# Kernel optimization log

Measured on AMD Instinct MI355X. Metric: run time of the kernel, lower is better.

Reference implementation:

```python
import jax, jax.numpy as jnp
import numpy as np

N_FEATURES = 32
HIDDEN_DIM = 64
B, T = 512, 1024


def lstm(x, w_ih, w_hh, b_ih, b_hh):
    """PyTorch-compatible single-layer LSTM, batch_first.
    x: [B, T, F_in]; w_ih: [4H, F_in]; w_hh: [4H, H]; b_ih, b_hh: [4H].
    Gate order (PyTorch): i, f, g, o. Returns outputs [B, T, H].
    """
    Bq, Tq, _ = x.shape
    H = w_hh.shape[1]
    # Precompute input contribution for all timesteps (big GEMM, time-parallel)
    x_gates = jnp.einsum('btf,gf->btg', x, w_ih) + b_ih + b_hh  # [B, T, 4H]
    x_gates = jnp.swapaxes(x_gates, 0, 1)  # [T, B, 4H]

    def step(carry, xg):
        h, c = carry
        gates = xg + h @ w_hh.T  # [B, 4H]
        i = jax.nn.sigmoid(gates[:, 0 * H:1 * H])
        f = jax.nn.sigmoid(gates[:, 1 * H:2 * H])
        g = jnp.tanh(gates[:, 2 * H:3 * H])
        o = jax.nn.sigmoid(gates[:, 3 * H:4 * H])
        c = f * c + i * g
        h = o * jnp.tanh(c)
        return (h, c), h

    h0 = jnp.zeros((Bq, H), dtype=x.dtype)
    c0 = jnp.zeros((Bq, H), dtype=x.dtype)
    _, hs = jax.lax.scan(step, (h0, c0), x_gates)  # hs: [T, B, H]
    return jnp.swapaxes(hs, 0, 1)  # [B, T, H]


def setup_inputs() -> dict:
    key = jax.random.key(0)
    ks = jax.random.split(key, 9)
    F, H = N_FEATURES, HIDDEN_DIM
    s_enc = 1.0 / np.sqrt(H)
    s_dec = 1.0 / np.sqrt(F)
    return {
        'x': jax.random.normal(ks[0], (B, T, F), dtype=jnp.float32),
        # encoder: input F -> hidden H
        'enc_w_ih': jax.random.uniform(ks[1], (4 * H, F), jnp.float32, -s_enc, s_enc),
        'enc_w_hh': jax.random.uniform(ks[2], (4 * H, H), jnp.float32, -s_enc, s_enc),
        'enc_b_ih': jax.random.uniform(ks[3], (4 * H,), jnp.float32, -s_enc, s_enc),
        'enc_b_hh': jax.random.uniform(ks[4], (4 * H,), jnp.float32, -s_enc, s_enc),
        # decoder: input H -> hidden F
        'dec_w_ih': jax.random.uniform(ks[5], (4 * F, H), jnp.float32, -s_dec, s_dec),
        'dec_w_hh': jax.random.uniform(ks[6], (4 * F, F), jnp.float32, -s_dec, s_dec),
        'dec_b_ih': jax.random.uniform(ks[7], (4 * F,), jnp.float32, -s_dec, s_dec),
        'dec_b_hh': jax.random.uniform(ks[8], (4 * F,), jnp.float32, -s_dec, s_dec),
    }


def reference(x, enc_w_ih, enc_w_hh, enc_b_ih, enc_b_hh,
              dec_w_ih, dec_w_hh, dec_b_ih, dec_b_hh):
    encoded = lstm(x, enc_w_ih, enc_w_hh, enc_b_ih, enc_b_hh)      # [B, T, H]
    decoded = lstm(encoded, dec_w_ih, dec_w_hh, dec_b_ih, dec_b_hh)  # [B, T, F]
    return decoded
```

## Files before the change

kernel.cpp:

```cpp
#include <hip/hip_runtime.h>
#include <stdint.h>
#include <math.h>

#define TT 1024
#define FF 32
#define HH 64

typedef unsigned int u32;
typedef _Float16 f16;
typedef __attribute__((ext_vector_type(8))) _Float16 half8;
typedef __attribute__((ext_vector_type(4))) float v4f;

__device__ __forceinline__ float fsig(float x) {
    return __builtin_amdgcn_rcpf(1.f + __builtin_amdgcn_exp2f(-1.44269504088896341f * x));
}
__device__ __forceinline__ float ftanh(float x) {
    return 2.f * __builtin_amdgcn_rcpf(1.f + __builtin_amdgcn_exp2f(-2.88539008177792681f * x)) - 1.f;
}

__device__ __forceinline__ half8 ld8h(const float* p) {
    float4 a = *(const float4*)p, b = *(const float4*)(p + 4);
    half8 r;
    r[0] = (f16)a.x; r[1] = (f16)a.y; r[2] = (f16)a.z; r[3] = (f16)a.w;
    r[4] = (f16)b.x; r[5] = (f16)b.y; r[6] = (f16)b.z; r[7] = (f16)b.w;
    return r;
}


__global__ __launch_bounds__(256, 2)
void lstm_ae_mfma(const float* __restrict__ x,
                  const float* __restrict__ ewih, const float* __restrict__ ewhh,
                  const float* __restrict__ ebih, const float* __restrict__ ebhh,
                  const float* __restrict__ dwih, const float* __restrict__ dwhh,
                  const float* __restrict__ dbih, const float* __restrict__ dbhh,
                  float* __restrict__ out)
{
    const int b = blockIdx.x;
    const int t = threadIdx.x;
    const int w = t >> 6;
    const int l = t & 63;
    const int q = l >> 4;
    const int n = l & 15;

    __shared__ __align__(16) f16 Bst[2][2][160];
    __shared__ __align__(16) float xst[2][2048];

    half8 af[6][3];
#pragma unroll
    for (int i = 0; i < 6; ++i) {
        int tile = w * 6 + i;
        if (tile < 16) {
            int r = (n & 3) * 64 + tile * 4 + (n >> 2);
            af[i][0] = ld8h(ewhh + r * 64 + q * 8);
            af[i][1] = ld8h(ewhh + r * 64 + 32 + q * 8);
            af[i][2] = ld8h(ewih + r * 32 + q * 8);
        } else {
            int r = (n & 3) * 32 + (tile - 16) * 4 + (n >> 2);
            af[i][0] = ld8h(dwih + r * 64 + q * 8);
            af[i][1] = ld8h(dwih + r * 64 + 32 + q * 8);
            af[i][2] = ld8h(dwhh + r * 32 + q * 8);
        }
    }

    const int sel = n >> 1;
    const bool act = (n < 12);
    const int tile_s = w * 6 + (sel < 6 ? sel : 0);
    const bool is_enc = (tile_s < 16);
    const int u = is_enc ? (tile_s * 4 + q) : ((tile_s - 16) * 4 + q);

    float b0 = 0.f, b1 = 0.f, b2 = 0.f, b3 = 0.f, c_st = 0.f;
    if (act) {
        if (is_enc) {
            b0 = ebih[u]       + ebhh[u];
            b1 = ebih[64 + u]  + ebhh[64 + u];
            b2 = ebih[128 + u] + ebhh[128 + u];
            b3 = ebih[192 + u] + ebhh[192 + u];
        } else {
            b0 = dbih[u]      + dbhh[u];
            b1 = dbih[32 + u] + dbhh[32 + u];
            b2 = dbih[64 + u] + dbhh[64 + u];
            b3 = dbih[96 + u] + dbhh[96 + u];
        }
    }

    { u32* bz = (u32*)&Bst[0][0][0]; for (int i2 = t; i2 < 2 * 2 * 160 / 2; i2 += 256) bz[i2] = 0u; }
    const float* xb = x + (size_t)b * TT * FF;
    *(float4*)&xst[0][t * 8]     = *(const float4*)(xb + t * 8);
    *(float4*)&xst[0][t * 8 + 4] = *(const float4*)(xb + t * 8 + 4);
    __syncthreads();
    if (t >= 96 && t < 128) Bst[0][0][64 + (t - 96)] = (f16)xst[0][t - 96];
    __syncthreads();

    for (int tt = 0; tt <= TT; ++tt) {
        const int p = tt & 1;

        float4 px0, px1;
        const int cn = (tt >> 6) + 1;
        const bool pf = ((tt & 63) == 0) && (cn < 16);
        if (pf) {
            px0 = *(const float4*)(xb + cn * 2048 + t * 8);
            px1 = *(const float4*)(xb + cn * 2048 + t * 8 + 4);
        }

        const f16* Bp = &Bst[p][0][0];
        const int cb = (n & 1) * 160 + q * 8;
        half8 bf0 = *(const half8*)(Bp + cb);
        half8 bf1 = *(const half8*)(Bp + cb + 32);
        half8 bf2 = *(const half8*)(Bp + cb + 64);
        half8 bf3 = *(const half8*)(Bp + cb + 96);

        v4f zero = {0.f, 0.f, 0.f, 0.f};
        v4f acc[6];
#pragma unroll
        for (int i = 0; i < 6; ++i) {
            const int tile = w * 6 + i;
            acc[i] = __builtin_amdgcn_mfma_f32_16x16x32_f16(af[i][2], (tile < 16) ? bf2 : bf3,
                                                            zero, 0, 0, 0);
        }
#pragma unroll
        for (int i = 0; i < 6; ++i)
            acc[i] = __builtin_amdgcn_mfma_f32_16x16x32_f16(af[i][0], bf0, acc[i], 0, 0, 0);
#pragma unroll
        for (int i = 0; i < 6; ++i)
            acc[i] = __builtin_amdgcn_mfma_f32_16x16x32_f16(af[i][1], bf1, acc[i], 0, 0, 0);

        v4f u_ = acc[0];
#pragma unroll
        for (int i = 1; i < 6; ++i) if (sel == i) u_ = acc[i];

        v4f s_;
#pragma unroll
        for (int e = 0; e < 4; ++e) {
            int tmp = __builtin_amdgcn_update_dpp(0, __float_as_int(u_[e]), 0xB1, 0xF, 0xF, true);
            s_[e] = u_[e] + __int_as_float(tmp);
        }

        f16* Bw = &Bst[p ^ 1][0][0];
        if (act && (is_enc ? (tt < TT) : (tt >= 1))) {
            float i_ = fsig(s_[0] + b0);
            float f_ = fsig(s_[1] + b1);
            float g_ = ftanh(s_[2] + b2);
            float o_ = fsig(s_[3] + b3);
            c_st = f_ * c_st + i_ * g_;
            float h = o_ * ftanh(c_st);
            f16 hi = (f16)h;
            f16 lo = (f16)(h - (float)hi);
            const int kk = is_enc ? u : (96 + u);
            Bw[(n & 1) * 160 + kk] = (n & 1) ? lo : hi;
            if (!is_enc && !(n & 1))
                out[(size_t)b * TT * FF + (size_t)(tt - 1) * FF + u] = h;
        } else if (n == 12 || n == 13) {
            int st = tt + 1;
            if (st < TT) {
                int j = w * 8 + q * 2 + (n - 12);
                Bw[64 + j] = (f16)xst[(st >> 6) & 1][(st & 63) * 32 + j];
            }
        }

        if (pf) {
            *(float4*)&xst[cn & 1][t * 8]     = px0;
            *(float4*)&xst[cn & 1][t * 8 + 4] = px1;
        }

        __syncthreads();
    }
}

extern "C" void kernel_launch(void* const* d_in, const int* in_sizes, int n_in,
                              void* d_out, int out_size, void* d_ws, size_t ws_size,
                              hipStream_t stream) {
    (void)in_sizes; (void)n_in; (void)out_size; (void)d_ws; (void)ws_size;
    lstm_ae_mfma<<<512, 256, 0, stream>>>((const float*)d_in[0],
                                          (const float*)d_in[1], (const float*)d_in[2],
                                          (const float*)d_in[3], (const float*)d_in[4],
                                          (const float*)d_in[5], (const float*)d_in[6],
                                          (const float*)d_in[7], (const float*)d_in[8],
                                          (float*)d_out);
}
```

Measured before the change: 740.8 us.

## Process two batch sequences per block by filling unused MFMA columns

Each block now runs two batch elements instead of one, using MFMA B-matrix columns that previously held only the hi/lo split of a single sequence (now 4 columns: 2 sequences x hi/lo). The grid is halved to 256 blocks and launch bounds drop to 1 block per CU, and each lane now evaluates up to two gate cells per step. This amortizes the per-step MFMA and barrier latency over twice the work, at the cost of fewer blocks, doubled per-lane activation math, and lower occupancy, since 256 blocks is about one per CU on the 256-CU MI355X.

```diff
diff --git a/kernel.cpp b/kernel.cpp
--- a/kernel.cpp
+++ b/kernel.cpp
@@ -5,6 +5,7 @@
 #define TT 1024
 #define FF 32
 #define HH 64
+#define CSTR 176
 
 typedef unsigned int u32;
 typedef _Float16 f16;
@@ -26,8 +27,13 @@
     return r;
 }
 
-
-__global__ __launch_bounds__(256, 2)
+__device__ __forceinline__ float pairsum(float v) {
+    int t = __builtin_amdgcn_update_dpp(0, __float_as_int(v), 0xB1, 0xF, 0xF, true);
+    return v + __int_as_float(t);
+}
+
+
+__global__ __launch_bounds__(256, 1)
 void lstm_ae_mfma(const float* __restrict__ x,
                   const float* __restrict__ ewih, const float* __restrict__ ewhh,
                   const float* __restrict__ ebih, const float* __restrict__ ebhh,
@@ -35,15 +41,15 @@
                   const float* __restrict__ dbih, const float* __restrict__ dbhh,
                   float* __restrict__ out)
 {
-    const int b = blockIdx.x;
+    const int b2 = blockIdx.x;
     const int t = threadIdx.x;
     const int w = t >> 6;
     const int l = t & 63;
     const int q = l >> 4;
     const int n = l & 15;
 
-    __shared__ __align__(16) f16 Bst[2][2][160];
-    __shared__ __align__(16) float xst[2][2048];
+    __shared__ __align__(16) f16 Bst[2][4][CSTR];
+    __shared__ __align__(16) float xst[2][2][2048];
 
     half8 af[6][3];
 #pragma unroll
@@ -62,48 +68,76 @@
         }
     }
 
-    const int sel = n >> 1;
-    const bool act = (n < 12);
-    const int tile_s = w * 6 + (sel < 6 ? sel : 0);
-    const bool is_enc = (tile_s < 16);
-    const int u = is_enc ? (tile_s * 4 + q) : ((tile_s - 16) * 4 + q);
-
-    float b0 = 0.f, b1 = 0.f, b2 = 0.f, b3 = 0.f, c_st = 0.f;
-    if (act) {
-        if (is_enc) {
-            b0 = ebih[u]       + ebhh[u];
-            b1 = ebih[64 + u]  + ebhh[64 + u];
-            b2 = ebih[128 + u] + ebhh[128 + u];
-            b3 = ebih[192 + u] + ebhh[192 + u];
+    const int pr   = n >> 1;
+    const int sq   = pr & 1;
+    const int slot = pr >> 1;
+    const int T1   = w * 6 + slot;
+    const bool e1  = (T1 < 16);
+    const int u1i  = e1 ? T1 * 4 + q : (T1 - 16) * 4 + q;
+    const bool has2 = (slot < 2);
+    const int T2   = w * 6 + 4 + slot;
+    const bool e2  = (T2 < 16);
+    const int u2i  = e2 ? T2 * 4 + q : (T2 - 16) * 4 + q;
+
+    const int wk1 = (sq * 2 + (n & 1)) * CSTR + (e1 ? u1i : 96 + u1i);
+    const int wk2 = (sq * 2 + (n & 1)) * CSTR + (e2 ? u2i : 96 + u2i);
+
+    float b10 = 0.f, b11 = 0.f, b12 = 0.f, b13 = 0.f, c1 = 0.f;
+    float b20 = 0.f, b21 = 0.f, b22 = 0.f, b23 = 0.f, c2 = 0.f;
+    if (e1) {
+        b10 = ebih[u1i]       + ebhh[u1i];
+        b11 = ebih[64 + u1i]  + ebhh[64 + u1i];
+        b12 = ebih[128 + u1i] + ebhh[128 + u1i];
+        b13 = ebih[192 + u1i] + ebhh[192 + u1i];
+    } else {
+        b10 = dbih[u1i]      + dbhh[u1i];
+        b11 = dbih[32 + u1i] + dbhh[32 + u1i];
+        b12 = dbih[64 + u1i] + dbhh[64 + u1i];
+        b13 = dbih[96 + u1i] + dbhh[96 + u1i];
+    }
+    if (has2) {
+        if (e2) {
+            b20 = ebih[u2i]       + ebhh[u2i];
+            b21 = ebih[64 + u2i]  + ebhh[64 + u2i];
+            b22 = ebih[128 + u2i] + ebhh[128 + u2i];
+            b23 = ebih[192 + u2i] + ebhh[192 + u2i];
         } else {
-            b0 = dbih[u]      + dbhh[u];
-            b1 = dbih[32 + u] + dbhh[32 + u];
-            b2 = dbih[64 + u] + dbhh[64 + u];
-            b3 = dbih[96 + u] + dbhh[96 + u];
-        }
-    }
-
-    { u32* bz = (u32*)&Bst[0][0][0]; for (int i2 = t; i2 < 2 * 2 * 160 / 2; i2 += 256) bz[i2] = 0u; }
-    const float* xb = x + (size_t)b * TT * FF;
-    *(float4*)&xst[0][t * 8]     = *(const float4*)(xb + t * 8);
-    *(float4*)&xst[0][t * 8 + 4] = *(const float4*)(xb + t * 8 + 4);
+            b20 = dbih[u2i]      + dbhh[u2i];
+            b21 = dbih[32 + u2i] + dbhh[32 + u2i];
+            b22 = dbih[64 + u2i] + dbhh[64 + u2i];
+            b23 = dbih[96 + u2i] + dbhh[96 + u2i];
+        }
+    }
+
+    { u32* bz = (u32*)&Bst[0][0][0]; for (int i2 = t; i2 < 2 * 4 * CSTR / 2; i2 += 256) bz[i2] = 0u; }
+    const float* xb0 = x + (size_t)(2 * b2) * TT * FF;
+    const float* xb1 = xb0 + TT * FF;
+    *(float4*)&xst[0][0][t * 8]     = *(const float4*)(xb0 + t * 8);
+    *(float4*)&xst[0][0][t * 8 + 4] = *(const float4*)(xb0 + t * 8 + 4);
+    *(float4*)&xst[1][0][t * 8]     = *(const float4*)(xb1 + t * 8);
+    *(float4*)&xst[1][0][t * 8 + 4] = *(const float4*)(xb1 + t * 8 + 4);
     __syncthreads();
-    if (t >= 96 && t < 128) Bst[0][0][64 + (t - 96)] = (f16)xst[0][t - 96];
+    if (t < 32)       Bst[0][0][64 + t]        = (f16)xst[0][0][t];
+    else if (t < 64)  Bst[0][2][64 + (t - 32)] = (f16)xst[1][0][t - 32];
     __syncthreads();
+
+    float* outp = out + (size_t)(2 * b2 + sq) * TT * FF;
 
     for (int tt = 0; tt <= TT; ++tt) {
         const int p = tt & 1;
 
-        float4 px0, px1;
+        float4 pa0, pa1, pb0, pb1;
         const int cn = (tt >> 6) + 1;
         const bool pf = ((tt & 63) == 0) && (cn < 16);
         if (pf) {
-            px0 = *(const float4*)(xb + cn * 2048 + t * 8);
-            px1 = *(const float4*)(xb + cn * 2048 + t * 8 + 4);
+            pa0 = *(const float4*)(xb0 + cn * 2048 + t * 8);
+            pa1 = *(const float4*)(xb0 + cn * 2048 + t * 8 + 4);
+            pb0 = *(const float4*)(xb1 + cn * 2048 + t * 8);
+            pb1 = *(const float4*)(xb1 + cn * 2048 + t * 8 + 4);
         }
 
         const f16* Bp = &Bst[p][0][0];
-        const int cb = (n & 1) * 160 + q * 8;
+        const int cb = (n & 3) * CSTR + q * 8;
         half8 bf0 = *(const half8*)(Bp + cb);
         half8 bf1 = *(const half8*)(Bp + cb + 32);
         half8 bf2 = *(const half8*)(Bp + cb + 64);
@@ -112,11 +146,9 @@
         v4f zero = {0.f, 0.f, 0.f, 0.f};
         v4f acc[6];
 #pragma unroll
-        for (int i = 0; i < 6; ++i) {
-            const int tile = w * 6 + i;
-            acc[i] = __builtin_amdgcn_mfma_f32_16x16x32_f16(af[i][2], (tile < 16) ? bf2 : bf3,
+        for (int i = 0; i < 6; ++i)
+            acc[i] = __builtin_amdgcn_mfma_f32_16x16x32_f16(af[i][2], (w * 6 + i < 16) ? bf2 : bf3,
                                                             zero, 0, 0, 0);
-        }
 #pragma unroll
         for (int i = 0; i < 6; ++i)
             acc[i] = __builtin_amdgcn_mfma_f32_16x16x32_f16(af[i][0], bf0, acc[i], 0, 0, 0);
@@ -124,42 +156,58 @@
         for (int i = 0; i < 6; ++i)
             acc[i] = __builtin_amdgcn_mfma_f32_16x16x32_f16(af[i][1], bf1, acc[i], 0, 0, 0);
 
-        v4f u_ = acc[0];
-#pragma unroll
-        for (int i = 1; i < 6; ++i) if (sel == i) u_ = acc[i];
-
-        v4f s_;
-#pragma unroll
-        for (int e = 0; e < 4; ++e) {
-            int tmp = __builtin_amdgcn_update_dpp(0, __float_as_int(u_[e]), 0xB1, 0xF, 0xF, true);
-            s_[e] = u_[e] + __int_as_float(tmp);
-        }
+        v4f u1 = acc[0];
+        if (slot == 1) u1 = acc[1];
+        if (slot == 2) u1 = acc[2];
+        if (slot == 3) u1 = acc[3];
+        v4f u2 = acc[4];
+        if (slot == 1) u2 = acc[5];
+
+        v4f s1, s2;
+#pragma unroll
+        for (int e = 0; e < 4; ++e) { s1[e] = pairsum(u1[e]); s2[e] = pairsum(u2[e]); }
 
         f16* Bw = &Bst[p ^ 1][0][0];
-        if (act && (is_enc ? (tt < TT) : (tt >= 1))) {
-            float i_ = fsig(s_[0] + b0);
-            float f_ = fsig(s_[1] + b1);
-            float g_ = ftanh(s_[2] + b2);
-            float o_ = fsig(s_[3] + b3);
-            c_st = f_ * c_st + i_ * g_;
-            float h = o_ * ftanh(c_st);
+
+        if (e1 ? (tt < TT) : (tt >= 1)) {
+            float i_ = fsig(s1[0] + b10);
+            float f_ = fsig(s1[1] + b11);
+            float g_ = ftanh(s1[2] + b12);
+            float o_ = fsig(s1[3] + b13);
+            c1 = f_ * c1 + i_ * g_;
+            float h = o_ * ftanh(c1);
             f16 hi = (f16)h;
             f16 lo = (f16)(h - (float)hi);
-            const int kk = is_enc ? u : (96 + u);
-            Bw[(n & 1) * 160 + kk] = (n & 1) ? lo : hi;
-            if (!is_enc && !(n & 1))
-                out[(size_t)b * TT * FF + (size_t)(tt - 1) * FF + u] = h;
-        } else if (n == 12 || n == 13) {
+            Bw[wk1] = (n & 1) ? lo : hi;
+            if (!e1 && !(n & 1)) outp[(size_t)(tt - 1) * FF + u1i] = h;
+        }
+        if (has2 && (e2 ? (tt < TT) : (tt >= 1))) {
+            float i_ = fsig(s2[0] + b20);
+            float f_ = fsig(s2[1] + b21);
+            float g_ = ftanh(s2[2] + b22);
+            float o_ = fsig(s2[3] + b23);
+            c2 = f_ * c2 + i_ * g_;
+            float h = o_ * ftanh(c2);
+            f16 hi = (f16)h;
+            f16 lo = (f16)(h - (float)hi);
+            Bw[wk2] = (n & 1) ? lo : hi;
+            if (!e2 && !(n & 1)) outp[(size_t)(tt - 1) * FF + u2i] = h;
+        }
+        if (n >= 12) {
             int st = tt + 1;
             if (st < TT) {
-                int j = w * 8 + q * 2 + (n - 12);
-                Bw[64 + j] = (f16)xst[(st >> 6) & 1][(st & 63) * 32 + j];
+                int idx = n - 12;
+                int sx = idx >> 1;
+                int jj = w * 8 + q * 2 + (idx & 1);
+                Bw[(sx * 2) * CSTR + 64 + jj] = (f16)xst[sx][(st >> 6) & 1][(st & 63) * 32 + jj];
             }
         }
 
         if (pf) {
-            *(float4*)&xst[cn & 1][t * 8]     = px0;
-            *(float4*)&xst[cn & 1][t * 8 + 4] = px1;
+            *(float4*)&xst[0][cn & 1][t * 8]     = pa0;
+            *(float4*)&xst[0][cn & 1][t * 8 + 4] = pa1;
+            *(float4*)&xst[1][cn & 1][t * 8]     = pb0;
+            *(float4*)&xst[1][cn & 1][t * 8 + 4] = pb1;
         }
 
         __syncthreads();
@@ -170,7 +218,7 @@
                               void* d_out, int out_size, void* d_ws, size_t ws_size,
                               hipStream_t stream) {
     (void)in_sizes; (void)n_in; (void)out_size; (void)d_ws; (void)ws_size;
-    lstm_ae_mfma<<<512, 256, 0, stream>>>((const float*)d_in[0],
+    lstm_ae_mfma<<<256, 256, 0, stream>>>((const float*)d_in[0],
                                           (const float*)d_in[1], (const float*)d_in[2],
                                           (const float*)d_in[3], (const float*)d_in[4],
                                           (const float*)d_in[5], (const float*)d_in[6],
```

New measurement: 1.606 ms. 117% more time.
